# Optimization experiments

Measured on AMD Instinct MI355X. Metric: run time of the kernel, lower is better.

## Reference

```python
import jax, jax.numpy as jnp
import numpy as np
import math

HEADS = 12

def setup_inputs() -> dict:
    key = jax.random.key(0)
    ks = jax.random.split(key, 5)
    E = 768
    r, i, n = 64, 256, 2
    s = 0.02  # init scale for weights
    return {
        "x": jax.random.normal(ks[0], (r, i, n, E), dtype=jnp.float32),
        "Wq": jax.random.normal(ks[1], (E, E), dtype=jnp.float32) * s,
        "bq": jnp.zeros((E,), dtype=jnp.float32),
        "Wk": jax.random.normal(ks[2], (E, E), dtype=jnp.float32) * s,
        "bk": jnp.zeros((E,), dtype=jnp.float32),
        "Wv": jax.random.normal(ks[3], (E, E), dtype=jnp.float32) * s,
        "bv": jnp.zeros((E,), dtype=jnp.float32),
        "Wo": jax.random.normal(ks[4], (E, E), dtype=jnp.float32) * s,
        "bo": jnp.zeros((E,), dtype=jnp.float32),
    }


def reference(x, Wq, bq, Wk, bk, Wv, bv, Wo, bo):
    r, i, n, E = x.shape
    h = HEADS
    d = E // h
    shape = (r, i, n, h, d)
    q = (x @ Wq + bq).reshape(shape)
    k = (x @ Wk + bk).reshape(shape)
    v = (x @ Wv + bv).reshape(shape)
    # tied row attention: 1/sqrt(d) softmax scale plus 1/sqrt(num_rows) for row sum
    scaling = d ** (-0.5) / math.sqrt(r)
    q = q * scaling
    # scores shared across all rows: contract over row axis r and head dim d
    attn_weights = jnp.einsum('rinhd,rjnhd->hnij', q, k)  # [h, n, i, j]
    attn_probs = jax.nn.softmax(attn_weights, axis=-1)
    # dropout disabled (deterministic=True)
    context = jnp.einsum('hnij,rjnhd->rinhd', attn_probs, v)
    context = context.reshape(r, i, n, E)
    return context @ Wo + bo
```

## Files before the change

kernel.cpp:

```cpp
#include <hip/hip_runtime.h>
#include <stdint.h>

typedef __attribute__((ext_vector_type(8))) short bf16x8;
typedef __attribute__((ext_vector_type(4))) float f32x4;
typedef __attribute__((ext_vector_type(4))) unsigned short us4;
typedef __attribute__((ext_vector_type(8))) unsigned short us8;

static __device__ __forceinline__ unsigned short f2bf(float f) {
  union { float f; unsigned u; } c; c.f = f;
  unsigned r = c.u + 0x7fffu + ((c.u >> 16) & 1u);
  return (unsigned short)(r >> 16);
}

static __device__ __forceinline__ void gl_lds16(const unsigned short* g, unsigned short* l) {
  __builtin_amdgcn_global_load_lds(
      (const __attribute__((address_space(1))) unsigned int*)g,
      (__attribute__((address_space(3))) unsigned int*)l, 16, 0, 0);
}

#define LDP 80

__device__ __forceinline__ void stage8(
    const unsigned short* __restrict__ Ag, int lda,
    const unsigned short* __restrict__ Bg, int ldb, int kt,
    unsigned short* As, unsigned short* Bs, int tid, int wid)
{
#pragma unroll
  for (int c = 0; c < 4; ++c) {
    int chunk = c * 256 + tid;
    int row = chunk >> 3, u = chunk & 7;
    int ch = u ^ (row & 7);
    gl_lds16(Ag + row * lda + kt + ch * 8, As + ((c * 256 + wid * 64) << 3));
    gl_lds16(Bg + row * ldb + kt + ch * 8, Bs + ((c * 256 + wid * 64) << 3));
  }
}

__device__ __forceinline__ void compute64(
    const unsigned short* As, const unsigned short* Bs, f32x4 acc[4][4],
    int wr, int wc, int lr, int kg, int l7)
{
#pragma unroll
  for (int ks = 0; ks < 2; ++ks) {
    bf16x8 af[4], bfr[4];
    int u = (ks * 4 + kg) ^ l7;
#pragma unroll
    for (int mi = 0; mi < 4; ++mi)
      af[mi] = *reinterpret_cast<const bf16x8*>(As + (wr*64 + mi*16 + lr) * 64 + u * 8);
#pragma unroll
    for (int ni = 0; ni < 4; ++ni)
      bfr[ni] = *reinterpret_cast<const bf16x8*>(Bs + (wc*64 + ni*16 + lr) * 64 + u * 8);
#pragma unroll
    for (int mi = 0; mi < 4; ++mi)
#pragma unroll
      for (int ni = 0; ni < 4; ++ni)
        acc[mi][ni] = __builtin_amdgcn_mfma_f32_16x16x32_bf16(af[mi], bfr[ni], acc[mi][ni], 0, 0, 0);
  }
}

__device__ __forceinline__ void gemm_core(
    const unsigned short* __restrict__ Ag, int lda,
    const unsigned short* __restrict__ Bg, int ldb,
    int K, unsigned short* As, unsigned short* Bs, f32x4 acc[4][4])
{
  const int tid  = threadIdx.x;
  const int lane = tid & 63;
  const int wid  = tid >> 6;
  const int wr = wid >> 1, wc = wid & 1;
  const int lr = lane & 15, kg = lane >> 4;
  const int l7 = lane & 7;

  const int nt = K >> 6;
  stage8(Ag, lda, Bg, ldb, 0, As, Bs, tid, wid);
  int cur = 0;
  for (int t = 0; t < nt - 1; ++t) {
    stage8(Ag, lda, Bg, ldb, (t + 1) << 6,
           As + (cur ^ 1) * 8192, Bs + (cur ^ 1) * 8192, tid, wid);
    asm volatile("s_waitcnt vmcnt(8)" ::: "memory");
    __builtin_amdgcn_s_barrier();
    compute64(As + cur * 8192, Bs + cur * 8192, acc, wr, wc, lr, kg, l7);
    __builtin_amdgcn_s_barrier();
    cur ^= 1;
  }
  asm volatile("s_waitcnt vmcnt(0)" ::: "memory");
  __builtin_amdgcn_s_barrier();
  compute64(As + cur * 8192, Bs + cur * 8192, acc, wr, wc, lr, kg, l7);
}

#define ACC_ZERO(acc) do { \
  f32x4 z = {0.f, 0.f, 0.f, 0.f}; \
  for (int a_ = 0; a_ < 4; ++a_) for (int b_ = 0; b_ < 4; ++b_) acc[a_][b_] = z; } while (0)

#define EPI_VARS \
  int tid = threadIdx.x, lane = tid & 63, wid = tid >> 6; \
  int wr = wid >> 1, wc = wid & 1, lr = lane & 15, kg = lane >> 4; (void)wr; (void)wc;

#define GEMM_LDS \
  __shared__ unsigned short As[2 * 128 * 64], Bs[2 * 128 * 64];


__global__ __launch_bounds__(256) void k_cvt_x(const float* __restrict__ x,
                                               unsigned short* __restrict__ xb) {
  int i = blockIdx.x * 256 + threadIdx.x;
  f32x4 f = reinterpret_cast<const f32x4*>(x)[i];
  us4 o = { f2bf(f[0]), f2bf(f[1]), f2bf(f[2]), f2bf(f[3]) };
  reinterpret_cast<us4*>(xb)[i] = o;
}

__global__ __launch_bounds__(256) void k_cvt_w(
    const float* __restrict__ Wq, const float* __restrict__ Wk, const float* __restrict__ Wv,
    const float* __restrict__ Wo, const float* __restrict__ bq, const float* __restrict__ bk,
    const float* __restrict__ bv, unsigned short* __restrict__ wT,
    unsigned short* __restrict__ woT, float* __restrict__ bqkv)
{
  const float qs = 1.0f / 64.0f;
  int o = blockIdx.x * 256 + threadIdx.x;
  if (o < 2304 * 768) {
    int col = o / 768, k = o % 768;
    float v;
    if (col < 768)       v = Wq[k * 768 + col] * qs;
    else if (col < 1536) v = Wk[k * 768 + col - 768];
    else                 v = Wv[k * 768 + col - 1536];
    wT[o] = f2bf(v);
  } else if (o < 2304 * 768 + 768 * 768) {
    int o2 = o - 2304 * 768;
    int col = o2 / 768, k = o2 % 768;
    woT[o2] = f2bf(Wo[k * 768 + col]);
  } else {
    int o3 = o - (2304 * 768 + 768 * 768);
    float v = (o3 < 768) ? bq[o3] * qs : (o3 < 1536 ? bk[o3 - 768] : bv[o3 - 1536]);
    bqkv[o3] = v;
  }
}

__global__ __launch_bounds__(256) void k_gemm_qkv(
    const unsigned short* __restrict__ xb, const unsigned short* __restrict__ wT,
    const float* __restrict__ bqkv, unsigned short* __restrict__ qkvb)
{
  GEMM_LDS;
  int bx = blockIdx.x, bn = bx % 18, bm = bx / 18;
  f32x4 acc[4][4]; ACC_ZERO(acc);
  gemm_core(xb + (size_t)bm * 128 * 768, 768, wT + (size_t)bn * 128 * 768, 768, 768, As, Bs, acc);
  EPI_VARS;
#pragma unroll
  for (int mi = 0; mi < 4; ++mi)
#pragma unroll
    for (int ni = 0; ni < 4; ++ni) {
      int col = bn * 128 + wc * 64 + ni * 16 + lr;
      float bias = bqkv[col];
#pragma unroll
      for (int e = 0; e < 4; ++e) {
        int row = bm * 128 + wr * 64 + mi * 16 + kg * 4 + e;
        qkvb[(size_t)row * 2304 + col] = f2bf(acc[mi][ni][e] + bias);
      }
    }
}

__global__ __launch_bounds__(256) void k_repack_v(
    const unsigned short* __restrict__ qkvb, unsigned short* __restrict__ V)
{
  __shared__ unsigned short lds[64 * LDP];
  int bx = blockIdx.x;
  int jt = bx & 3, rr = (bx >> 2) & 63, hn = bx >> 8;
  int h = hn >> 1, nn = hn & 1;
  int t = threadIdx.x;
  int j = t >> 3, ch = t & 7;
#pragma unroll
  for (int p = 0; p < 2; ++p) {
    int jj = p * 32 + j;
    us8 v = *reinterpret_cast<const us8*>(
        qkvb + ((size_t)((rr * 256 + jt * 64 + jj) * 2 + nn)) * 2304 + 1536 + h * 64 + ch * 8);
#pragma unroll
    for (int e = 0; e < 8; ++e) lds[(ch * 8 + e) * LDP + jj] = v[e];
  }
  __syncthreads();
  int dd = t >> 2, cj = t & 3;
  size_t ob = ((size_t)(hn * 64 + rr) * 64) * 256;
#pragma unroll
  for (int p = 0; p < 2; ++p) {
    int c2 = cj + p * 4;
    us8 v = *reinterpret_cast<const us8*>(lds + dd * LDP + c2 * 8);
    *reinterpret_cast<us8*>(V + ob + (size_t)dd * 256 + jt * 64 + c2 * 8) = v;
  }
}

__global__ __launch_bounds__(256) void k_gemm_scores(
    const unsigned short* __restrict__ qkvb, float* __restrict__ Spart)
{
  __shared__ unsigned short Asp[128 * LDP], Bsp[128 * LDP];
  int bx = blockIdx.x;
  int s = bx / 96, rblk = bx % 96;
  int hn = rblk >> 2, tt = rblk & 3, bm = tt >> 1, bn = tt & 1;
  int h = hn >> 1, nn = hn & 1;
  const int hq = h * 64;
  f32x4 acc[4][4]; ACC_ZERO(acc);

  const int tid = threadIdx.x, lane = tid & 63, wid = tid >> 6;
  const int wr = wid >> 1, wc = wid & 1, lr = lane & 15, kg = lane >> 4;
  const int srow = tid >> 3, sch = tid & 7;

  for (int t = 0; t < 16; ++t) {
    int rr = s * 16 + t;
    us8 av[4], bv[4];
#pragma unroll
    for (int c = 0; c < 4; ++c) {
      int row = c * 32 + srow;
      size_t ab = ((size_t)((rr * 256 + bm * 128 + row) * 2 + nn)) * 2304 + hq + sch * 8;
      size_t bb = ((size_t)((rr * 256 + bn * 128 + row) * 2 + nn)) * 2304 + 768 + hq + sch * 8;
      av[c] = *reinterpret_cast<const us8*>(qkvb + ab);
      bv[c] = *reinterpret_cast<const us8*>(qkvb + bb);
    }
    __syncthreads();
#pragma unroll
    for (int c = 0; c < 4; ++c) {
      int row = c * 32 + srow;
      *reinterpret_cast<us8*>(Asp + row * LDP + sch * 8) = av[c];
      *reinterpret_cast<us8*>(Bsp + row * LDP + sch * 8) = bv[c];
    }
    __syncthreads();
#pragma unroll
    for (int ks = 0; ks < 2; ++ks) {
      bf16x8 af[4], bfr[4];
#pragma unroll
      for (int mi = 0; mi < 4; ++mi)
        af[mi] = *reinterpret_cast<const bf16x8*>(Asp + (wr*64 + mi*16 + lr) * LDP + ks*32 + kg*8);
#pragma unroll
      for (int ni = 0; ni < 4; ++ni)
        bfr[ni] = *reinterpret_cast<const bf16x8*>(Bsp + (wc*64 + ni*16 + lr) * LDP + ks*32 + kg*8);
#pragma unroll
      for (int mi = 0; mi < 4; ++mi)
#pragma unroll
        for (int ni = 0; ni < 4; ++ni)
          acc[mi][ni] = __builtin_amdgcn_mfma_f32_16x16x32_bf16(af[mi], bfr[ni], acc[mi][ni], 0, 0, 0);
    }
  }

  float* Ss = Spart + ((size_t)s * 24 + hn) * 65536;
#pragma unroll
  for (int mi = 0; mi < 4; ++mi)
#pragma unroll
    for (int ni = 0; ni < 4; ++ni)
#pragma unroll
      for (int e = 0; e < 4; ++e) {
        int row = bm * 128 + wr * 64 + mi * 16 + kg * 4 + e;
        int col = bn * 128 + wc * 64 + ni * 16 + lr;
        Ss[(size_t)row * 256 + col] = acc[mi][ni][e];
      }
}

__global__ __launch_bounds__(256) void k_softmax(const float* __restrict__ Sp,
                                                 unsigned short* __restrict__ P)
{
  __shared__ float red[8];
  size_t row = blockIdx.x;
  int t = threadIdx.x, wid = t >> 6, lane = t & 63;
  size_t idx = row * 256 + t;
  float v = Sp[idx] + Sp[idx + 1572864] + Sp[idx + 2 * 1572864] + Sp[idx + 3 * 1572864];
  float m = v;
#pragma unroll
  for (int o = 32; o; o >>= 1) m = fmaxf(m, __shfl_xor(m, o));
  if (lane == 0) red[wid] = m;
  __syncthreads();
  m = fmaxf(fmaxf(red[0], red[1]), fmaxf(red[2], red[3]));
  float e = __expf(v - m);
  float sm = e;
#pragma unroll
  for (int o = 32; o; o >>= 1) sm += __shfl_xor(sm, o);
  if (lane == 0) red[4 + wid] = sm;
  __syncthreads();
  sm = red[4] + red[5] + red[6] + red[7];
  P[row * 256 + t] = f2bf(e / sm);
}

__global__ __launch_bounds__(256) void k_gemm_ctx(
    const unsigned short* __restrict__ P, const unsigned short* __restrict__ V,
    unsigned short* __restrict__ Cb)
{
  GEMM_LDS;
  int bx = blockIdx.x;
  int hn = bx / 64, tt = bx % 64, bm = tt >> 5, bn = tt & 31;
  f32x4 acc[4][4]; ACC_ZERO(acc);
  const unsigned short* Ag = P + (size_t)hn * 65536 + (size_t)bm * 128 * 256;
  const unsigned short* Bg = V + (size_t)hn * 4096 * 256 + (size_t)bn * 128 * 256;
  gemm_core(Ag, 256, Bg, 256, 256, As, Bs, acc);
  EPI_VARS;
  int nn = hn & 1;
  int h = hn >> 1;
#pragma unroll
  for (int mi = 0; mi < 4; ++mi)
#pragma unroll
    for (int ni = 0; ni < 4; ++ni) {
      int c = bn * 128 + wc * 64 + ni * 16 + lr;
      int rr = c >> 6, dd = c & 63;
#pragma unroll
      for (int e = 0; e < 4; ++e) {
        int i = bm * 128 + wr * 64 + mi * 16 + kg * 4 + e;
        int tok = (rr * 256 + i) * 2 + nn;
        Cb[(size_t)tok * 768 + h * 64 + dd] = f2bf(acc[mi][ni][e]);
      }
    }
}

__global__ __launch_bounds__(256) void k_gemm_out(
    const unsigned short* __restrict__ Cb, const unsigned short* __restrict__ woT,
    const float* __restrict__ bo, float* __restrict__ out)
{
  GEMM_LDS;
  int b0 = blockIdx.x;
  int bx = (b0 & 7) * 192 + (b0 >> 3);
  int bn = bx % 6, bm = bx / 6;
  f32x4 acc[4][4]; ACC_ZERO(acc);
  gemm_core(Cb + (size_t)bm * 128 * 768, 768, woT + (size_t)bn * 128 * 768, 768, 768, As, Bs, acc);
  EPI_VARS;
#pragma unroll
  for (int mi = 0; mi < 4; ++mi)
#pragma unroll
    for (int ni = 0; ni < 4; ++ni) {
      int col = bn * 128 + wc * 64 + ni * 16 + lr;
      float bias = bo[col];
#pragma unroll
      for (int e = 0; e < 4; ++e) {
        int row = bm * 128 + wr * 64 + mi * 16 + kg * 4 + e;
        out[(size_t)row * 768 + col] = acc[mi][ni][e] + bias;
      }
    }
}

extern "C" void kernel_launch(void* const* d_in, const int* in_sizes, int n_in,
                              void* d_out, int out_size, void* d_ws, size_t ws_size,
                              hipStream_t stream)
{
  const float* x  = (const float*)d_in[0];
  const float* Wq = (const float*)d_in[1];
  const float* bq = (const float*)d_in[2];
  const float* Wk = (const float*)d_in[3];
  const float* bk = (const float*)d_in[4];
  const float* Wv = (const float*)d_in[5];
  const float* bv = (const float*)d_in[6];
  const float* Wo = (const float*)d_in[7];
  const float* bo = (const float*)d_in[8];
  float* out = (float*)d_out;

  char* ws = (char*)d_ws;
  size_t off = 0;
  auto alloc = [&](size_t bytes) { void* p = ws + off; off += (bytes + 255) & ~(size_t)255; return p; };
  unsigned short* xb   = (unsigned short*)alloc(50331648);
  unsigned short* qkvb = (unsigned short*)alloc(150994944);
  unsigned short* Vb   = (unsigned short*)alloc(50331648);
  unsigned short* Cb   = (unsigned short*)alloc(50331648);
  unsigned short* wT   = (unsigned short*)alloc(3538944);
  unsigned short* woT  = (unsigned short*)alloc(1179648);
  float*          bqkv = (float*)alloc(9216);
  if (off > ws_size) return;

  float*          Sp = (float*)d_out;
  unsigned short* P  = (unsigned short*)((char*)d_out + 25165824);

  k_cvt_x      <<<24576, 256, 0, stream>>>(x, xb);
  k_cvt_w      <<<9225,  256, 0, stream>>>(Wq, Wk, Wv, Wo, bq, bk, bv, wT, woT, bqkv);
  k_gemm_qkv   <<<4608,  256, 0, stream>>>(xb, wT, bqkv, qkvb);
  k_repack_v   <<<6144,  256, 0, stream>>>(qkvb, Vb);
  k_gemm_scores<<<384,   256, 0, stream>>>(qkvb, Sp);
  k_softmax    <<<6144,  256, 0, stream>>>(Sp, P);
  k_gemm_ctx   <<<1536,  256, 0, stream>>>(P, Vb, Cb);
  k_gemm_out   <<<1536,  256, 0, stream>>>(Cb, woT, bo, out);
}
```

Measured before the change: 352.6 us.

## Use 256x256 tiles with 512 threads for QKV and output projection GEMMs

Adds a 256x256-tile GEMM core run by 8 waves, with a double-buffered LDS pipeline that interleaves global-to-LDS staging of the next K tile with the MFMA work. It also raises wave priority around the MFMA bursts. The QKV and output projection kernels switch to this core to get more arithmetic reuse per byte loaded and fewer blocks. In exchange each thread holds twice the accumulator registers and the kernel uses 128KB of LDS per block, which limits occupancy. The output GEMM also loses its block swizzle and now launches only 384 blocks, which may leave CUs idle in the tail.

```diff
diff --git a/kernel.cpp b/kernel.cpp
--- a/kernel.cpp
+++ b/kernel.cpp
@@ -19,6 +19,72 @@
 }
 
 #define LDP 80
+
+#define QT 16384
+
+__device__ __forceinline__ void gemm256_core(
+    const unsigned short* __restrict__ Ag, int lda,
+    const unsigned short* __restrict__ Bg, int ldb,
+    int K, unsigned short* As, unsigned short* Bs, f32x4 acc[8][4])
+{
+  const int tid  = threadIdx.x;
+  const int lane = tid & 63;
+  const int wid  = tid >> 6;
+  const int wr = wid >> 2, wc = wid & 3;
+  const int lr = lane & 15, kg = lane >> 4;
+  const int l7 = lane & 7;
+  const int srow = tid >> 3;
+  const int sch  = (tid & 7) ^ (srow & 7);
+
+  auto STG = [&](int c, int kt, int bufo) {
+    int row = c * 64 + srow;
+    gl_lds16(Ag + row * lda + kt + sch * 8, As + bufo + ((c * 512 + wid * 64) << 3));
+    gl_lds16(Bg + row * ldb + kt + sch * 8, Bs + bufo + ((c * 512 + wid * 64) << 3));
+  };
+
+  const int nt = K >> 6;
+  STG(0, 0, 0); STG(1, 0, 0); STG(2, 0, 0); STG(3, 0, 0);
+  int cur = 0;
+  for (int t = 0; t < nt; ++t) {
+    const bool last = (t == nt - 1);
+    const int kt1 = (t + 1) << 6;
+    const int cb = cur * QT, nb = (cur ^ 1) * QT;
+    if (!last) STG(0, kt1, nb);
+    if (last) asm volatile("s_waitcnt vmcnt(0)" ::: "memory");
+    else      asm volatile("s_waitcnt vmcnt(2)" ::: "memory");
+    __builtin_amdgcn_s_barrier();
+    bf16x8 bf[4][2];
+#pragma unroll
+    for (int ni = 0; ni < 4; ++ni)
+#pragma unroll
+      for (int ks = 0; ks < 2; ++ks)
+        bf[ni][ks] = *reinterpret_cast<const bf16x8*>(
+            Bs + cb + (wc*64 + ni*16 + lr) * 64 + (((ks*4 + kg) ^ l7) << 3));
+#pragma unroll
+    for (int q = 0; q < 4; ++q) {
+      bf16x8 af[2][2];
+#pragma unroll
+      for (int m2 = 0; m2 < 2; ++m2)
+#pragma unroll
+        for (int ks = 0; ks < 2; ++ks)
+          af[m2][ks] = *reinterpret_cast<const bf16x8*>(
+              As + cb + (wr*128 + (q*2 + m2)*16 + lr) * 64 + (((ks*4 + kg) ^ l7) << 3));
+      if (!last && q < 3) STG(q + 1, kt1, nb);
+      __builtin_amdgcn_s_setprio(1);
+#pragma unroll
+      for (int ks = 0; ks < 2; ++ks)
+#pragma unroll
+        for (int m2 = 0; m2 < 2; ++m2)
+#pragma unroll
+          for (int ni = 0; ni < 4; ++ni)
+            acc[q*2 + m2][ni] = __builtin_amdgcn_mfma_f32_16x16x32_bf16(
+                af[m2][ks], bf[ni][ks], acc[q*2 + m2][ni], 0, 0, 0);
+      __builtin_amdgcn_s_setprio(0);
+    }
+    __builtin_amdgcn_s_barrier();
+    cur ^= 1;
+  }
+}
 
 __device__ __forceinline__ void stage8(
     const unsigned short* __restrict__ Ag, int lda,
@@ -89,6 +155,10 @@
 #define ACC_ZERO(acc) do { \
   f32x4 z = {0.f, 0.f, 0.f, 0.f}; \
   for (int a_ = 0; a_ < 4; ++a_) for (int b_ = 0; b_ < 4; ++b_) acc[a_][b_] = z; } while (0)
+
+#define ACC_ZERO8(acc) do { \
+  f32x4 z = {0.f, 0.f, 0.f, 0.f}; \
+  for (int a_ = 0; a_ < 8; ++a_) for (int b_ = 0; b_ < 4; ++b_) acc[a_][b_] = z; } while (0)
 
 #define EPI_VARS \
   int tid = threadIdx.x, lane = tid & 63, wid = tid >> 6; \
@@ -132,24 +202,26 @@
   }
 }
 
-__global__ __launch_bounds__(256) void k_gemm_qkv(
+__global__ __launch_bounds__(512, 2) void k_gemm_qkv(
     const unsigned short* __restrict__ xb, const unsigned short* __restrict__ wT,
     const float* __restrict__ bqkv, unsigned short* __restrict__ qkvb)
 {
-  GEMM_LDS;
-  int bx = blockIdx.x, bn = bx % 18, bm = bx / 18;
-  f32x4 acc[4][4]; ACC_ZERO(acc);
-  gemm_core(xb + (size_t)bm * 128 * 768, 768, wT + (size_t)bn * 128 * 768, 768, 768, As, Bs, acc);
-  EPI_VARS;
-#pragma unroll
-  for (int mi = 0; mi < 4; ++mi)
+  __shared__ unsigned short As[2 * QT], Bs[2 * QT];
+  int bx = blockIdx.x, bn = bx % 9, bm = bx / 9;
+  f32x4 acc[8][4]; ACC_ZERO8(acc);
+  gemm256_core(xb + (size_t)bm * 256 * 768, 768, wT + (size_t)bn * 256 * 768, 768,
+               768, As, Bs, acc);
+  const int lane = threadIdx.x & 63, wid = threadIdx.x >> 6;
+  const int wr = wid >> 2, wc = wid & 3, lr = lane & 15, kg = lane >> 4;
+#pragma unroll
+  for (int mi = 0; mi < 8; ++mi)
 #pragma unroll
     for (int ni = 0; ni < 4; ++ni) {
-      int col = bn * 128 + wc * 64 + ni * 16 + lr;
+      int col = bn * 256 + wc * 64 + ni * 16 + lr;
       float bias = bqkv[col];
 #pragma unroll
       for (int e = 0; e < 4; ++e) {
-        int row = bm * 128 + wr * 64 + mi * 16 + kg * 4 + e;
+        int row = bm * 256 + wr * 128 + mi * 16 + kg * 4 + e;
         qkvb[(size_t)row * 2304 + col] = f2bf(acc[mi][ni][e] + bias);
       }
     }
@@ -300,26 +372,26 @@
     }
 }
 
-__global__ __launch_bounds__(256) void k_gemm_out(
+__global__ __launch_bounds__(512, 2) void k_gemm_out(
     const unsigned short* __restrict__ Cb, const unsigned short* __restrict__ woT,
     const float* __restrict__ bo, float* __restrict__ out)
 {
-  GEMM_LDS;
-  int b0 = blockIdx.x;
-  int bx = (b0 & 7) * 192 + (b0 >> 3);
-  int bn = bx % 6, bm = bx / 6;
-  f32x4 acc[4][4]; ACC_ZERO(acc);
-  gemm_core(Cb + (size_t)bm * 128 * 768, 768, woT + (size_t)bn * 128 * 768, 768, 768, As, Bs, acc);
-  EPI_VARS;
-#pragma unroll
-  for (int mi = 0; mi < 4; ++mi)
+  __shared__ unsigned short As[2 * QT], Bs[2 * QT];
+  int bx = blockIdx.x, bn = bx % 3, bm = bx / 3;
+  f32x4 acc[8][4]; ACC_ZERO8(acc);
+  gemm256_core(Cb + (size_t)bm * 256 * 768, 768, woT + (size_t)bn * 256 * 768, 768,
+               768, As, Bs, acc);
+  const int lane = threadIdx.x & 63, wid = threadIdx.x >> 6;
+  const int wr = wid >> 2, wc = wid & 3, lr = lane & 15, kg = lane >> 4;
+#pragma unroll
+  for (int mi = 0; mi < 8; ++mi)
 #pragma unroll
     for (int ni = 0; ni < 4; ++ni) {
-      int col = bn * 128 + wc * 64 + ni * 16 + lr;
+      int col = bn * 256 + wc * 64 + ni * 16 + lr;
       float bias = bo[col];
 #pragma unroll
       for (int e = 0; e < 4; ++e) {
-        int row = bm * 128 + wr * 64 + mi * 16 + kg * 4 + e;
+        int row = bm * 256 + wr * 128 + mi * 16 + kg * 4 + e;
         out[(size_t)row * 768 + col] = acc[mi][ni][e] + bias;
       }
     }
@@ -357,10 +429,10 @@
 
   k_cvt_x      <<<24576, 256, 0, stream>>>(x, xb);
   k_cvt_w      <<<9225,  256, 0, stream>>>(Wq, Wk, Wv, Wo, bq, bk, bv, wT, woT, bqkv);
-  k_gemm_qkv   <<<4608,  256, 0, stream>>>(xb, wT, bqkv, qkvb);
+  k_gemm_qkv   <<<1152,  512, 0, stream>>>(xb, wT, bqkv, qkvb);
   k_repack_v   <<<6144,  256, 0, stream>>>(qkvb, Vb);
   k_gemm_scores<<<384,   256, 0, stream>>>(qkvb, Sp);
   k_softmax    <<<6144,  256, 0, stream>>>(Sp, P);
   k_gemm_ctx   <<<1536,  256, 0, stream>>>(P, Vb, Cb);
-  k_gemm_out   <<<1536,  256, 0, stream>>>(Cb, woT, bo, out);
-}
+  k_gemm_out   <<<384,   512, 0, stream>>>(Cb, woT, bo, out);
+}
```

Result: slower. 366.5 us (+3.9%).
